# Performance work log

Hardware: AMD Instinct MI355X
Metric: run time of the kernel (lower is better)

## Reference

```python
import jax, jax.numpy as jnp
import numpy as np

N = 20000
E = 320000
NEG_SLOPE = 0.2
BN_EPS = 1e-5


def _segment_softmax(e, dst, n):
    # e: [E, H] attention logits, dst: [E] destination node ids
    m = jax.ops.segment_max(e, dst, num_segments=n)           # [N, H]
    ex = jnp.exp(e - m[dst])                                   # [E, H]
    s = jax.ops.segment_sum(ex, dst, num_segments=n)          # [N, H]
    return ex / s[dst]


def gat_conv(x, src, dst, W, a_src, a_dst, b, heads, out_ch):
    # PyG GATConv (concat=True): h = x @ W reshaped to [N, H, C]
    n = x.shape[0]
    h = (x @ W).reshape(n, heads, out_ch)                      # [N, H, C]
    al_s = jnp.einsum('nhc,hc->nh', h, a_src)                  # [N, H]
    al_d = jnp.einsum('nhc,hc->nh', h, a_dst)
    e = jax.nn.leaky_relu(al_s[src] + al_d[dst], NEG_SLOPE)    # [E, H]
    alpha = _segment_softmax(e, dst, n)                        # [E, H]
    msg = h[src] * alpha[:, :, None]                           # [E, H, C]
    out = jax.ops.segment_sum(msg, dst, num_segments=n)        # [N, H, C]
    return out.reshape(n, heads * out_ch) + b


def batch_norm(x, gamma, beta):
    mu = jnp.mean(x, axis=0)
    var = jnp.mean((x - mu) ** 2, axis=0)  # biased, as torch BN training
    return gamma * (x - mu) * jax.lax.rsqrt(var + BN_EPS) + beta


def setup_inputs() -> dict:
    key = jax.random.key(0)
    ks = jax.random.split(key, 16)
    F_in, H1, C1 = 128, 8, 64
    D = H1 * C1  # 512
    OUT = 2
    def gl(k, shape, fan):
        return jax.random.normal(k, shape, dtype=jnp.float32) / np.sqrt(fan)
    x = jax.random.normal(ks[0], (N, F_in), dtype=jnp.float32)
    edge_index = jax.random.randint(ks[1], (2, E), 0, N, dtype=jnp.int64)
    return {
        'x': x, 'edge_index': edge_index,
        'W1': gl(ks[2], (F_in, H1 * C1), F_in),
        'a1s': gl(ks[3], (H1, C1), C1), 'a1d': gl(ks[4], (H1, C1), C1),
        'b1': jnp.zeros((D,), jnp.float32),
        'W2': gl(ks[5], (D, D), D),
        'a2s': gl(ks[6], (1, D), D), 'a2d': gl(ks[7], (1, D), D),
        'b2': jnp.zeros((D,), jnp.float32),
        'fc1_w': gl(ks[8], (D, D), D), 'fc1_b': jnp.zeros((D,), jnp.float32),
        'g1': jnp.ones((D,), jnp.float32), 'be1': jnp.zeros((D,), jnp.float32),
        'fc2_w': gl(ks[9], (D, D), D), 'fc2_b': jnp.zeros((D,), jnp.float32),
        'g2': jnp.ones((D,), jnp.float32), 'be2': jnp.zeros((D,), jnp.float32),
        'lin_w': gl(ks[10], (D, OUT), D), 'lin_b': jnp.zeros((OUT,), jnp.float32),
    }


def reference(x, edge_index, W1, a1s, a1d, b1, W2, a2s, a2d, b2,
              fc1_w, fc1_b, g1, be1, fc2_w, fc2_b, g2, be2, lin_w, lin_b):
    n = x.shape[0]
    loop = jnp.arange(n, dtype=edge_index.dtype)
    src = jnp.concatenate([edge_index[0], loop])  # add self-loops (PyG default)
    dst = jnp.concatenate([edge_index[1], loop])
    h = gat_conv(x, src, dst, W1, a1s, a1d, b1, heads=8, out_ch=64)
    h = batch_norm(jax.nn.relu(h @ fc1_w + fc1_b), g1, be1)
    h = gat_conv(h, src, dst, W2, a2s, a2d, b2, heads=1, out_ch=512)
    h = batch_norm(jax.nn.relu(h @ fc2_w + fc2_b), g2, be2)
    out = jax.nn.relu(h @ lin_w + lin_b)  # dropout p=0 is identity
    return out
```

## Files before the change

kernel.cpp:

```cpp
#include <hip/hip_runtime.h>
#include <hip/hip_bf16.h>

static constexpr int NN = 20000;
static constexpr int EE = 320000;
static constexpr int ET = EE + NN;
static constexpr int DD = 512;
static constexpr int FIN = 128;

typedef __attribute__((ext_vector_type(8))) short short8;
typedef __attribute__((ext_vector_type(4))) float f32x4;

__device__ __forceinline__ unsigned short f2bf(float f) {
    unsigned u = __float_as_uint(f);
    u += 0x7fffu + ((u >> 16) & 1u);
    return (unsigned short)(u >> 16);
}
__device__ __forceinline__ float bf2f(unsigned short b) {
    return __uint_as_float(((unsigned)b) << 16);
}

__device__ __forceinline__ void async_copy16(short* lds, const unsigned short* g) {
    __builtin_amdgcn_global_load_lds(
        (const __attribute__((address_space(1))) unsigned int*)g,
        (__attribute__((address_space(3))) unsigned int*)lds,
        16, 0, 0);
}

__global__ void init_k(int* __restrict__ deg, int* __restrict__ cursor,
                       const unsigned* __restrict__ ei, int* __restrict__ flag) {
    int i = blockIdx.x * blockDim.x + threadIdx.x;
    if (i < NN) { deg[i] = 1; cursor[i] = 0; }
    if (i == 0) {
        int is64 = 1;
        for (int j = 0; j < 64; ++j)
            if (ei[2 * j + 1] != 0u) { is64 = 0; break; }
        *flag = is64;
    }
}

__global__ void convert_idx(const void* __restrict__ ei, const int* __restrict__ flag,
                            int* __restrict__ src32, int* __restrict__ dst32,
                            int* __restrict__ deg) {
    int i = blockIdx.x * blockDim.x + threadIdx.x;
    if (i >= EE) return;
    int s, d;
    if (*flag) {
        const long long* p = (const long long*)ei;
        s = (int)p[i]; d = (int)p[EE + i];
    } else {
        const int* p = (const int*)ei;
        s = p[i]; d = p[EE + i];
    }
    src32[i] = s;
    dst32[i] = d;
    atomicAdd(&deg[d], 1);
}

__global__ void scan_k(const int* __restrict__ deg, int* __restrict__ row_ptr) {
    __shared__ int part[1024];
    int t = threadIdx.x;
    const int CH = (NN + 1023) / 1024;
    int start = t * CH;
    int end = min(start + CH, NN);
    int s = 0;
    for (int i = start; i < end; ++i) s += deg[i];
    part[t] = s;
    __syncthreads();
    for (int off = 1; off < 1024; off <<= 1) {
        int v = 0;
        if (t >= off) v = part[t - off];
        __syncthreads();
        part[t] += v;
        __syncthreads();
    }
    int base = (t == 0) ? 0 : part[t - 1];
    for (int i = start; i < end; ++i) { row_ptr[i] = base; base += deg[i]; }
    if (t == 1023) row_ptr[NN] = part[1023];
}

__global__ void fill_csr(const int* __restrict__ src, const int* __restrict__ dst,
                         const int* __restrict__ row_ptr, int* __restrict__ cursor,
                         int* __restrict__ csr_src) {
    int e = blockIdx.x * blockDim.x + threadIdx.x;
    if (e >= ET) return;
    int d = (e < EE) ? dst[e] : (e - EE);
    int s = (e < EE) ? src[e] : (e - EE);
    int pos = atomicAdd(&cursor[d], 1);
    csr_src[row_ptr[d] + pos] = s;
}

static constexpr int SZ_X  = NN * FIN;
static constexpr int SZ_W1 = FIN * DD;
static constexpr int SZ_W  = DD * DD;
static constexpr int SZ_Z  = 2 * 1024 + 2 * NN;
__global__ void prep_k(const float* __restrict__ x, const float* __restrict__ W1,
                       const float* __restrict__ fc1, const float* __restrict__ W2,
                       const float* __restrict__ fc2,
                       unsigned short* __restrict__ xb, unsigned short* __restrict__ W1t,
                       unsigned short* __restrict__ fc1t, unsigned short* __restrict__ W2t,
                       unsigned short* __restrict__ fc2t,
                       float* __restrict__ bnstatA, float* __restrict__ bnstatB,
                       float* __restrict__ al_s2, float* __restrict__ al_d2) {
    int i = blockIdx.x * blockDim.x + threadIdx.x;
    if (i < SZ_X) { xb[i] = f2bf(x[i]); return; }
    i -= SZ_X;
    if (i < SZ_W1) {
        int k = i / DD, n = i - k * DD;
        W1t[(size_t)n * FIN + k] = f2bf(W1[i]);
        return;
    }
    i -= SZ_W1;
    if (i < 3 * SZ_W) {
        const float* Wp; unsigned short* Tp;
        if (i < SZ_W) { Wp = fc1; Tp = fc1t; }
        else if (i < 2 * SZ_W) { i -= SZ_W; Wp = W2; Tp = W2t; }
        else { i -= 2 * SZ_W; Wp = fc2; Tp = fc2t; }
        int k = i / DD, n = i - k * DD;
        Tp[(size_t)n * DD + k] = f2bf(Wp[i]);
        return;
    }
    i -= 3 * SZ_W;
    if (i < 1024) { bnstatA[i] = 0.f; return; }
    i -= 1024;
    if (i < 1024) { bnstatB[i] = 0.f; return; }
    i -= 1024;
    if (i < NN) { al_s2[i] = 0.f; return; }
    i -= NN;
    if (i < NN) { al_d2[i] = 0.f; return; }
}

template <int RELU, int HASBIAS, int STATS, int ALS, int H>
__global__ __launch_bounds__(256) void gemm_bf16(const unsigned short* __restrict__ A,
                                                 const unsigned short* __restrict__ Bt,
                                                 const float* __restrict__ bias,
                                                 unsigned short* __restrict__ Cb,
                                                 float* __restrict__ bnstat,
                                                 const float* __restrict__ avs,
                                                 const float* __restrict__ avd,
                                                 float* __restrict__ al_s,
                                                 float* __restrict__ al_d,
                                                 int M, int Nc, int K) {
    __shared__ short As0[128 * 32], As1[128 * 32];
    __shared__ short Bs0[128 * 32], Bs1[128 * 32];
    int t = threadIdx.x;
    int m0 = blockIdx.y * 128, n0 = blockIdx.x * 128;
    int lane = t & 63, w = t >> 6;
    int wm = w & 1, wn = w >> 1;
    int quad = lane >> 4, mr = lane & 15;
    int lrow = lane >> 2;
    int lcol = (lane & 3) * 8;

    const unsigned short* Ag0 = A + (size_t)(m0 + w * 32 + lrow) * K + lcol;
    const unsigned short* Ag1 = A + (size_t)(m0 + w * 32 + 16 + lrow) * K + lcol;
    const unsigned short* Bg0 = Bt + (size_t)(n0 + w * 32 + lrow) * K + lcol;
    const unsigned short* Bg1 = Bt + (size_t)(n0 + w * 32 + 16 + lrow) * K + lcol;
    short* Al[2][2] = {{&As0[(w * 32) * 32], &As0[(w * 32 + 16) * 32]},
                       {&As1[(w * 32) * 32], &As1[(w * 32 + 16) * 32]}};
    short* Bl[2][2] = {{&Bs0[(w * 32) * 32], &Bs0[(w * 32 + 16) * 32]},
                       {&Bs1[(w * 32) * 32], &Bs1[(w * 32 + 16) * 32]}};

    f32x4 zero = {0.f, 0.f, 0.f, 0.f};
    f32x4 acc[4][4];
#pragma unroll
    for (int i = 0; i < 4; ++i)
#pragma unroll
        for (int j = 0; j < 4; ++j) acc[i][j] = zero;

    for (int k0 = 0; k0 < K; k0 += 64) {
        async_copy16(Al[0][0], Ag0 + k0);
        async_copy16(Al[1][0], Ag0 + k0 + 32);
        async_copy16(Al[0][1], Ag1 + k0);
        async_copy16(Al[1][1], Ag1 + k0 + 32);
        async_copy16(Bl[0][0], Bg0 + k0);
        async_copy16(Bl[1][0], Bg0 + k0 + 32);
        async_copy16(Bl[0][1], Bg1 + k0);
        async_copy16(Bl[1][1], Bg1 + k0 + 32);
        __syncthreads();
#pragma unroll
        for (int kp = 0; kp < 2; ++kp) {
            const short* Sa = kp ? As1 : As0;
            const short* Sb = kp ? Bs1 : Bs0;
            short8 af[4], bfr[4];
#pragma unroll
            for (int i = 0; i < 4; ++i) {
                af[i]  = *(const short8*)(&Sa[(wm * 64 + i * 16 + mr) * 32 + quad * 8]);
                bfr[i] = *(const short8*)(&Sb[(wn * 64 + i * 16 + mr) * 32 + quad * 8]);
            }
#pragma unroll
            for (int i = 0; i < 4; ++i)
#pragma unroll
                for (int j = 0; j < 4; ++j)
                    acc[i][j] = __builtin_amdgcn_mfma_f32_16x16x32_bf16(af[i], bfr[j], acc[i][j], 0, 0, 0);
        }
        __syncthreads();
    }

    float as_j[4], ad_j[4];
    if (ALS) {
#pragma unroll
        for (int j = 0; j < 4; ++j) {
            int n = n0 + wn * 64 + j * 16 + mr;
            as_j[j] = avs[n];
            ad_j[j] = avd[n];
        }
    }
    const int head = (H == 8) ? ((n0 + wn * 64) >> 6) : 0;
    float sj[4] = {0.f, 0.f, 0.f, 0.f}, qj[4] = {0.f, 0.f, 0.f, 0.f};
#pragma unroll
    for (int i = 0; i < 4; ++i) {
        int mb = m0 + wm * 64 + i * 16 + quad * 4;
#pragma unroll
        for (int r = 0; r < 4; ++r) {
            int m = mb + r;
            bool valid = (m < M);
            float ps = 0.f, pd = 0.f;
#pragma unroll
            for (int j = 0; j < 4; ++j) {
                int n = n0 + wn * 64 + j * 16 + mr;
                float v = acc[i][j][r];
                if (HASBIAS) v += bias[n];
                if (RELU) v = fmaxf(v, 0.f);
                unsigned short hb = f2bf(v);
                if (valid) Cb[(size_t)m * Nc + n] = hb;
                if (ALS) {
                    float vv = bf2f(hb);
                    ps += as_j[j] * vv;
                    pd += ad_j[j] * vv;
                }
                if (STATS && valid) { sj[j] += v; qj[j] += v * v; }
            }
            if (ALS) {
                ps += __shfl_xor(ps, 1); pd += __shfl_xor(pd, 1);
                ps += __shfl_xor(ps, 2); pd += __shfl_xor(pd, 2);
                ps += __shfl_xor(ps, 4); pd += __shfl_xor(pd, 4);
                ps += __shfl_xor(ps, 8); pd += __shfl_xor(pd, 8);
                if (mr == 0 && valid) {
                    if (H == 8) { al_s[m * 8 + head] = ps; al_d[m * 8 + head] = pd; }
                    else        { atomicAdd(&al_s[m], ps); atomicAdd(&al_d[m], pd); }
                }
            }
        }
    }
    if (STATS) {
#pragma unroll
        for (int j = 0; j < 4; ++j) {
            float s = sj[j], q = qj[j];
            s += __shfl_xor(s, 16); q += __shfl_xor(q, 16);
            s += __shfl_xor(s, 32); q += __shfl_xor(q, 32);
            if (lane < 16) {
                int n = n0 + wn * 64 + j * 16 + mr;
                atomicAdd(&bnstat[n], s);
                atomicAdd(&bnstat[512 + n], q);
            }
        }
    }
}

template <int H>
__global__ __launch_bounds__(256) void gat_gather_k(const unsigned short* __restrict__ hb,
                                                    const float* __restrict__ al_s,
                                                    const float* __restrict__ al_d,
                                                    const int* __restrict__ row_ptr,
                                                    const int* __restrict__ csr_src,
                                                    const float* __restrict__ bias,
                                                    unsigned short* __restrict__ outb) {
    int t = threadIdx.x;
    int w = t >> 6, lane = t & 63;
    int n = blockIdx.x * 4 + w;
    int beg = row_ptr[n], end = row_ptr[n + 1];
    const int hh = (H == 8) ? (lane >> 3) : 0;
    float ald = al_d[n * H + hh];
    float psum = 0.f;
    float acc[8] = {0.f, 0.f, 0.f, 0.f, 0.f, 0.f, 0.f, 0.f};

    for (int p0 = beg; p0 < end; p0 += 64) {
        int cnt = min(64, end - p0);
        int sv = (p0 + lane < end) ? csr_src[p0 + lane] : 0;
        int p = 0;
        for (; p + 8 <= cnt; p += 8) {
            int sn[8];
#pragma unroll
            for (int u = 0; u < 8; ++u) sn[u] = __shfl(sv, p + u);
            float l[8];
#pragma unroll
            for (int u = 0; u < 8; ++u) l[u] = al_s[sn[u] * H + hh] + ald;
            short8 hv[8];
#pragma unroll
            for (int u = 0; u < 8; ++u)
                hv[u] = *(const short8*)(hb + (size_t)sn[u] * DD + lane * 8);
            float a[8];
#pragma unroll
            for (int u = 0; u < 8; ++u) {
                float x = l[u];
                a[u] = __expf((x > 0.f) ? x : 0.2f * x);
                psum += a[u];
            }
#pragma unroll
            for (int u = 0; u < 8; ++u)
#pragma unroll
                for (int j = 0; j < 8; ++j) acc[j] += a[u] * bf2f((unsigned short)hv[u][j]);
        }
        for (; p < cnt; ++p) {
            int sn0 = __shfl(sv, p);
            float l0 = al_s[sn0 * H + hh] + ald;
            short8 h0 = *(const short8*)(hb + (size_t)sn0 * DD + lane * 8);
            float a0 = __expf((l0 > 0.f) ? l0 : 0.2f * l0);
            psum += a0;
#pragma unroll
            for (int j = 0; j < 8; ++j) acc[j] += a0 * bf2f((unsigned short)h0[j]);
        }
    }
    float inv = 1.0f / psum;
    unsigned short ov[8];
#pragma unroll
    for (int j = 0; j < 8; ++j) ov[j] = f2bf(acc[j] * inv + bias[lane * 8 + j]);
    *(int4*)(outb + (size_t)n * DD + lane * 8) = *(const int4*)ov;
}

__global__ __launch_bounds__(256) void fold1_k(const float* __restrict__ stat,
                                               const float* __restrict__ g,
                                               const float* __restrict__ be,
                                               unsigned short* __restrict__ W2t,
                                               float* __restrict__ bias2) {
    int t = threadIdx.x;
    int n = blockIdx.x * 4 + (t >> 6);
    int lane = t & 63;
    float pb = 0.f;
#pragma unroll
    for (int j = 0; j < 8; ++j) {
        int k = lane * 8 + j;
        float mean = stat[k] * (1.0f / NN);
        float var = stat[512 + k] * (1.0f / NN) - mean * mean;
        float sc = g[k] * rsqrtf(var + 1e-5f);
        float sh = be[k] - mean * sc;
        float wv = bf2f(W2t[n * DD + k]);
        W2t[n * DD + k] = f2bf(sc * wv);
        pb += sh * wv;
    }
    for (int off = 32; off; off >>= 1) pb += __shfl_down(pb, off);
    if (lane == 0) bias2[n] = pb;
}

__global__ void fold_k(const float* __restrict__ stat, const float* __restrict__ g,
                       const float* __restrict__ be, const float* __restrict__ w,
                       const float* __restrict__ b, float* __restrict__ wfold,
                       float* __restrict__ bfold) {
    __shared__ float r0[512], r1[512];
    int c = threadIdx.x;
    float mean = stat[c] * (1.0f / NN);
    float var = stat[512 + c] * (1.0f / NN) - mean * mean;
    float sc = g[c] * rsqrtf(var + 1e-5f);
    float sh = be[c] - mean * sc;
    float w0 = w[2 * c], w1 = w[2 * c + 1];
    wfold[2 * c] = sc * w0;
    wfold[2 * c + 1] = sc * w1;
    r0[c] = sh * w0;
    r1[c] = sh * w1;
    __syncthreads();
    for (int off = 256; off; off >>= 1) {
        if (c < off) { r0[c] += r0[c + off]; r1[c] += r1[c + off]; }
        __syncthreads();
    }
    if (c == 0) { bfold[0] = r0[0] + b[0]; bfold[1] = r1[0] + b[1]; }
}

__global__ void final_linear(const unsigned short* __restrict__ xb, const float* __restrict__ w,
                             const float* __restrict__ b, float* __restrict__ out) {
    int wave = (blockIdx.x * blockDim.x + threadIdx.x) >> 6;
    int lane = threadIdx.x & 63;
    if (wave >= NN) return;
    short8 hv = *(const short8*)(xb + (size_t)wave * DD + lane * 8);
    float p0 = 0.f, p1 = 0.f;
#pragma unroll
    for (int j = 0; j < 8; ++j) {
        int c = lane * 8 + j;
        float v = bf2f((unsigned short)hv[j]);
        p0 += v * w[2 * c];
        p1 += v * w[2 * c + 1];
    }
    for (int off = 32; off; off >>= 1) {
        p0 += __shfl_down(p0, off);
        p1 += __shfl_down(p1, off);
    }
    if (lane == 0) {
        out[wave * 2 + 0] = fmaxf(p0 + b[0], 0.f);
        out[wave * 2 + 1] = fmaxf(p1 + b[1], 0.f);
    }
}

extern "C" void kernel_launch(void* const* d_in, const int* in_sizes, int n_in,
                              void* d_out, int out_size, void* d_ws, size_t ws_size,
                              hipStream_t stream) {
    const float* x     = (const float*)d_in[0];
    const void*  ei    = d_in[1];
    const float* W1    = (const float*)d_in[2];
    const float* a1s   = (const float*)d_in[3];
    const float* a1d   = (const float*)d_in[4];
    const float* b1    = (const float*)d_in[5];
    const float* W2    = (const float*)d_in[6];
    const float* a2s   = (const float*)d_in[7];
    const float* a2d   = (const float*)d_in[8];
    const float* b2    = (const float*)d_in[9];
    const float* fc1_w = (const float*)d_in[10];
    const float* fc1_b = (const float*)d_in[11];
    const float* g1    = (const float*)d_in[12];
    const float* be1   = (const float*)d_in[13];
    const float* fc2_w = (const float*)d_in[14];
    const float* fc2_b = (const float*)d_in[15];
    const float* g2    = (const float*)d_in[16];
    const float* be2   = (const float*)d_in[17];
    const float* lin_w = (const float*)d_in[18];
    const float* lin_b = (const float*)d_in[19];
    float* out = (float*)d_out;

    char* ws = (char*)d_ws;
    auto alloc = [&](size_t bytes) {
        void* p = (void*)ws;
        ws += (bytes + 255) & ~size_t(255);
        return p;
    };
    unsigned short* h_bf    = (unsigned short*)alloc((size_t)NN * DD * 2);
    unsigned short* act_bf  = (unsigned short*)alloc((size_t)NN * DD * 2);
    unsigned short* W1t     = (unsigned short*)alloc((size_t)DD * FIN * 2);
    unsigned short* fc1t    = (unsigned short*)alloc((size_t)DD * DD * 2);
    unsigned short* W2t     = (unsigned short*)alloc((size_t)DD * DD * 2);
    unsigned short* fc2t    = (unsigned short*)alloc((size_t)DD * DD * 2);
    float*          al_s    = (float*)alloc((size_t)NN * 8 * 4);
    float*          al_d    = (float*)alloc((size_t)NN * 8 * 4);
    float*          al_s2   = (float*)alloc((size_t)NN * 4);
    float*          al_d2   = (float*)alloc((size_t)NN * 4);
    int*            row_ptr = (int*)alloc((size_t)(NN + 1) * 4);
    int*            deg     = (int*)alloc((size_t)NN * 4);
    int*            cursor  = (int*)alloc((size_t)NN * 4);
    int*            csr_src = (int*)alloc((size_t)ET * 4);
    int*            src32   = (int*)alloc((size_t)EE * 4);
    int*            dst32   = (int*)alloc((size_t)EE * 4);
    int*            flag    = (int*)alloc(256);
    float*          bnstatA = (float*)alloc(1024 * 4);
    float*          bnstatB = (float*)alloc(1024 * 4);
    float*          bias2f  = (float*)alloc(512 * 4);
    float*          wfold   = (float*)alloc(1024 * 4);
    float*          bfold   = (float*)alloc(256);

    init_k<<<(NN + 255) / 256, 256, 0, stream>>>(deg, cursor, (const unsigned*)ei, flag);
    convert_idx<<<(EE + 255) / 256, 256, 0, stream>>>(ei, flag, src32, dst32, deg);
    scan_k<<<1, 1024, 0, stream>>>(deg, row_ptr);
    fill_csr<<<(ET + 255) / 256, 256, 0, stream>>>(src32, dst32, row_ptr, cursor, csr_src);

    unsigned short* x_bf = act_bf;
    const int prep_total = SZ_X + SZ_W1 + 3 * SZ_W + SZ_Z;
    prep_k<<<(prep_total + 255) / 256, 256, 0, stream>>>(x, W1, fc1_w, W2, fc2_w,
                                                         x_bf, W1t, fc1t, W2t, fc2t,
                                                         bnstatA, bnstatB, al_s2, al_d2);

    dim3 gg(DD / 128, (NN + 127) / 128);

    gemm_bf16<0, 0, 0, 1, 8><<<gg, 256, 0, stream>>>(
        x_bf, W1t, nullptr, h_bf, nullptr, a1s, a1d, al_s, al_d, NN, DD, FIN);
    gat_gather_k<8><<<NN / 4, 256, 0, stream>>>(h_bf, al_s, al_d, row_ptr, csr_src, b1, act_bf);
    gemm_bf16<1, 1, 1, 0, 8><<<gg, 256, 0, stream>>>(
        act_bf, fc1t, fc1_b, h_bf, bnstatA, nullptr, nullptr, nullptr, nullptr, NN, DD, DD);
    fold1_k<<<128, 256, 0, stream>>>(bnstatA, g1, be1, W2t, bias2f);

    gemm_bf16<0, 1, 0, 1, 1><<<gg, 256, 0, stream>>>(
        h_bf, W2t, bias2f, act_bf, nullptr, a2s, a2d, al_s2, al_d2, NN, DD, DD);
    gat_gather_k<1><<<NN / 4, 256, 0, stream>>>(act_bf, al_s2, al_d2, row_ptr, csr_src, b2, h_bf);
    gemm_bf16<1, 1, 1, 0, 8><<<gg, 256, 0, stream>>>(
        h_bf, fc2t, fc2_b, act_bf, bnstatB, nullptr, nullptr, nullptr, nullptr, NN, DD, DD);

    fold_k<<<1, 512, 0, stream>>>(bnstatB, g2, be2, lin_w, lin_b, wfold, bfold);
    final_linear<<<(NN + 3) / 4, 256, 0, stream>>>(act_bf, wfold, bfold, out);
}
```

Before: 375.3 us.

## Double-buffer GEMM k-loop with async prefetch and tile weight transposes

The GEMM main loop now uses ping-pong LDS buffers with 32-wide k steps. The next k-slice is issued asynchronously while MFMAs run on the current one, so each iteration needs one barrier instead of two. Separately, the weight transpose and bf16 conversion move out of the elementwise prep kernel into a shared-memory tiled transpose kernel, so the global writes are coalesced. The risk is that the async loads into the next buffer rely on an implicit wait at the barrier, and the smaller k step means more iterations and more barriers overall.

Result: no change. 379.7 us (+1.2%).

```diff
diff --git a/kernel.cpp b/kernel.cpp
--- a/kernel.cpp
+++ b/kernel.cpp
@@ -89,37 +89,42 @@
     csr_src[row_ptr[d] + pos] = s;
 }
 
-static constexpr int SZ_X  = NN * FIN;
-static constexpr int SZ_W1 = FIN * DD;
-static constexpr int SZ_W  = DD * DD;
-static constexpr int SZ_Z  = 2 * 1024 + 2 * NN;
-__global__ void prep_k(const float* __restrict__ x, const float* __restrict__ W1,
-                       const float* __restrict__ fc1, const float* __restrict__ W2,
-                       const float* __restrict__ fc2,
-                       unsigned short* __restrict__ xb, unsigned short* __restrict__ W1t,
-                       unsigned short* __restrict__ fc1t, unsigned short* __restrict__ W2t,
-                       unsigned short* __restrict__ fc2t,
+__global__ __launch_bounds__(256) void transpose_w_k(
+    const float* __restrict__ W1, const float* __restrict__ fc1,
+    const float* __restrict__ W2, const float* __restrict__ fc2,
+    unsigned short* __restrict__ W1t, unsigned short* __restrict__ fc1t,
+    unsigned short* __restrict__ W2t, unsigned short* __restrict__ fc2t) {
+    __shared__ unsigned short tile[64][65];
+    int b = blockIdx.x;
+    const float* src; unsigned short* dst; int rows, cols;
+    if (b < 16)       { src = W1;  dst = W1t;  rows = FIN; cols = DD; }
+    else if (b < 80)  { b -= 16;  src = fc1; dst = fc1t; rows = DD; cols = DD; }
+    else if (b < 144) { b -= 80;  src = W2;  dst = W2t;  rows = DD; cols = DD; }
+    else              { b -= 144; src = fc2; dst = fc2t; rows = DD; cols = DD; }
+    int tc = cols / 64;
+    int r0 = (b / tc) * 64, c0 = (b % tc) * 64;
+    int t = threadIdx.x, lr = t >> 6, lc = t & 63;
+#pragma unroll
+    for (int p = 0; p < 16; ++p) {
+        int r = lr + p * 4;
+        tile[r][lc] = f2bf(src[(size_t)(r0 + r) * cols + c0 + lc]);
+    }
+    __syncthreads();
+#pragma unroll
+    for (int p = 0; p < 16; ++p) {
+        int r = lr + p * 4;
+        dst[(size_t)(c0 + r) * rows + r0 + lc] = tile[lc][r];
+    }
+}
+
+static constexpr int SZ_X = NN * FIN;
+static constexpr int SZ_Z = 2 * 1024 + 2 * NN;
+__global__ void prep_k(const float* __restrict__ x, unsigned short* __restrict__ xb,
                        float* __restrict__ bnstatA, float* __restrict__ bnstatB,
                        float* __restrict__ al_s2, float* __restrict__ al_d2) {
     int i = blockIdx.x * blockDim.x + threadIdx.x;
     if (i < SZ_X) { xb[i] = f2bf(x[i]); return; }
     i -= SZ_X;
-    if (i < SZ_W1) {
-        int k = i / DD, n = i - k * DD;
-        W1t[(size_t)n * FIN + k] = f2bf(W1[i]);
-        return;
-    }
-    i -= SZ_W1;
-    if (i < 3 * SZ_W) {
-        const float* Wp; unsigned short* Tp;
-        if (i < SZ_W) { Wp = fc1; Tp = fc1t; }
-        else if (i < 2 * SZ_W) { i -= SZ_W; Wp = W2; Tp = W2t; }
-        else { i -= 2 * SZ_W; Wp = fc2; Tp = fc2t; }
-        int k = i / DD, n = i - k * DD;
-        Tp[(size_t)n * DD + k] = f2bf(Wp[i]);
-        return;
-    }
-    i -= 3 * SZ_W;
     if (i < 1024) { bnstatA[i] = 0.f; return; }
     i -= 1024;
     if (i < 1024) { bnstatB[i] = 0.f; return; }
@@ -140,8 +145,8 @@
                                                  float* __restrict__ al_s,
                                                  float* __restrict__ al_d,
                                                  int M, int Nc, int K) {
-    __shared__ short As0[128 * 32], As1[128 * 32];
-    __shared__ short Bs0[128 * 32], Bs1[128 * 32];
+    __shared__ short As[2][128 * 32];
+    __shared__ short Bs[2][128 * 32];
     int t = threadIdx.x;
     int m0 = blockIdx.y * 128, n0 = blockIdx.x * 128;
     int lane = t & 63, w = t >> 6;
@@ -154,10 +159,7 @@
     const unsigned short* Ag1 = A + (size_t)(m0 + w * 32 + 16 + lrow) * K + lcol;
     const unsigned short* Bg0 = Bt + (size_t)(n0 + w * 32 + lrow) * K + lcol;
     const unsigned short* Bg1 = Bt + (size_t)(n0 + w * 32 + 16 + lrow) * K + lcol;
-    short* Al[2][2] = {{&As0[(w * 32) * 32], &As0[(w * 32 + 16) * 32]},
-                       {&As1[(w * 32) * 32], &As1[(w * 32 + 16) * 32]}};
-    short* Bl[2][2] = {{&Bs0[(w * 32) * 32], &Bs0[(w * 32 + 16) * 32]},
-                       {&Bs1[(w * 32) * 32], &Bs1[(w * 32 + 16) * 32]}};
+    const int la0 = (w * 32) * 32, la1 = (w * 32 + 16) * 32;
 
     f32x4 zero = {0.f, 0.f, 0.f, 0.f};
     f32x4 acc[4][4];
@@ -166,33 +168,34 @@
 #pragma unroll
         for (int j = 0; j < 4; ++j) acc[i][j] = zero;
 
-    for (int k0 = 0; k0 < K; k0 += 64) {
-        async_copy16(Al[0][0], Ag0 + k0);
-        async_copy16(Al[1][0], Ag0 + k0 + 32);
-        async_copy16(Al[0][1], Ag1 + k0);
-        async_copy16(Al[1][1], Ag1 + k0 + 32);
-        async_copy16(Bl[0][0], Bg0 + k0);
-        async_copy16(Bl[1][0], Bg0 + k0 + 32);
-        async_copy16(Bl[0][1], Bg1 + k0);
-        async_copy16(Bl[1][1], Bg1 + k0 + 32);
+    async_copy16(&As[0][la0], Ag0);
+    async_copy16(&As[0][la1], Ag1);
+    async_copy16(&Bs[0][la0], Bg0);
+    async_copy16(&Bs[0][la1], Bg1);
+
+    const int nk = K >> 5;
+    for (int kk = 0; kk < nk; ++kk) {
+        int cur = kk & 1;
         __syncthreads();
-#pragma unroll
-        for (int kp = 0; kp < 2; ++kp) {
-            const short* Sa = kp ? As1 : As0;
-            const short* Sb = kp ? Bs1 : Bs0;
-            short8 af[4], bfr[4];
-#pragma unroll
-            for (int i = 0; i < 4; ++i) {
-                af[i]  = *(const short8*)(&Sa[(wm * 64 + i * 16 + mr) * 32 + quad * 8]);
-                bfr[i] = *(const short8*)(&Sb[(wn * 64 + i * 16 + mr) * 32 + quad * 8]);
-            }
-#pragma unroll
-            for (int i = 0; i < 4; ++i)
-#pragma unroll
-                for (int j = 0; j < 4; ++j)
-                    acc[i][j] = __builtin_amdgcn_mfma_f32_16x16x32_bf16(af[i], bfr[j], acc[i][j], 0, 0, 0);
-        }
-        __syncthreads();
+        if (kk + 1 < nk) {
+            int kof = (kk + 1) << 5;
+            int nxt = cur ^ 1;
+            async_copy16(&As[nxt][la0], Ag0 + kof);
+            async_copy16(&As[nxt][la1], Ag1 + kof);
+            async_copy16(&Bs[nxt][la0], Bg0 + kof);
+            async_copy16(&Bs[nxt][la1], Bg1 + kof);
+        }
+        short8 af[4], bfr[4];
+#pragma unroll
+        for (int i = 0; i < 4; ++i) {
+            af[i]  = *(const short8*)(&As[cur][(wm * 64 + i * 16 + mr) * 32 + quad * 8]);
+            bfr[i] = *(const short8*)(&Bs[cur][(wn * 64 + i * 16 + mr) * 32 + quad * 8]);
+        }
+#pragma unroll
+        for (int i = 0; i < 4; ++i)
+#pragma unroll
+            for (int j = 0; j < 4; ++j)
+                acc[i][j] = __builtin_amdgcn_mfma_f32_16x16x32_bf16(af[i], bfr[j], acc[i][j], 0, 0, 0);
     }
 
     float as_j[4], ad_j[4];
@@ -448,10 +451,8 @@
     fill_csr<<<(ET + 255) / 256, 256, 0, stream>>>(src32, dst32, row_ptr, cursor, csr_src);
 
     unsigned short* x_bf = act_bf;
-    const int prep_total = SZ_X + SZ_W1 + 3 * SZ_W + SZ_Z;
-    prep_k<<<(prep_total + 255) / 256, 256, 0, stream>>>(x, W1, fc1_w, W2, fc2_w,
-                                                         x_bf, W1t, fc1t, W2t, fc2t,
-                                                         bnstatA, bnstatB, al_s2, al_d2);
+    transpose_w_k<<<208, 256, 0, stream>>>(W1, fc1_w, W2, fc2_w, W1t, fc1t, W2t, fc2t);
+    prep_k<<<(SZ_X + SZ_Z + 255) / 256, 256, 0, stream>>>(x, x_bf, bnstatA, bnstatB, al_s2, al_d2);
 
     dim3 gg(DD / 128, (NN + 127) / 128);
 
```
